# Kernel tuning notes

Measured on AMD Instinct MI355X. Metric: run time of the kernel, lower is better.

Reference implementation:

```python
import jax, jax.numpy as jnp
import numpy as np

NUM_HEADS = 12  # matches init_kwargs num_heads


def dwconv(x, w, b, groups):
    # depthwise conv, NHWC, SAME padding, stride 1 (DepthwiseConv2D in source)
    y = jax.lax.conv_general_dilated(x, w, (1, 1), 'SAME', (1, 1), (1, 1),
                                     ('NHWC', 'HWIO', 'NHWC'), groups)
    return y + b


def setup_inputs() -> dict:
    key = jax.random.key(0)
    ks = jax.random.split(key, 6)
    B, N, C = 16, 1025, 768  # N = 1 + 32*32
    inputs = jax.random.normal(ks[0], (B, N, C), jnp.float32)
    cpe_w = jax.random.normal(ks[1], (3, 3, 1, C), jnp.float32) * 0.05   # ConvPosEnc 3x3 depthwise
    cpe_b = jnp.zeros((C,), jnp.float32)
    w_qkv = jax.random.normal(ks[2], (C, 3 * C), jnp.float32) * 0.02     # Dense(dim*3, use_bias=False)
    crpe_w = jax.random.normal(ks[3], (1, 1, 1, C), jnp.float32) * 0.05  # ConvRelPosEnc window=1 depthwise
    crpe_b = jnp.zeros((C,), jnp.float32)
    w_proj = jax.random.normal(ks[4], (C, C), jnp.float32) * 0.02        # Dense(dim)
    b_proj = jnp.zeros((C,), jnp.float32)
    return {'inputs': inputs, 'cpe_w': cpe_w, 'cpe_b': cpe_b, 'w_qkv': w_qkv,
            'crpe_w': crpe_w, 'crpe_b': crpe_b, 'w_proj': w_proj, 'b_proj': b_proj}


def reference(inputs, cpe_w, cpe_b, w_qkv, crpe_w, crpe_b, w_proj, b_proj):
    B, N, C = inputs.shape
    H = W = int((N - 1) ** 0.5)
    nh = NUM_HEADS
    dh = C // nh
    scale = dh ** (-0.5)

    # ConvPosEnc: depthwise 3x3 conv on image tokens + residual, cls token passes through
    cls_tok, img = inputs[:, :1], inputs[:, 1:]
    feat = img.reshape(B, H, W, C)
    x = dwconv(feat, cpe_w, cpe_b, C) + feat
    pe = jnp.concatenate([cls_tok, x.reshape(B, H * W, C)], axis=1)  # [B,N,C]

    # qkv projection (no bias)
    qkv = (pe @ w_qkv).reshape(B, N, 3, nh, dh)
    qkv = jnp.transpose(qkv, (2, 0, 3, 1, 4))  # [3,B,nh,N,dh]
    q, k, v = qkv[0], qkv[1], qkv[2]

    # factorized (linear) attention: softmax over tokens on K, then two einsums
    k_soft = jax.nn.softmax(k, axis=2)
    kTv = jnp.einsum('bhnk,bhnv->bhkv', k_soft, v)       # [B,nh,dh,dh]
    factor_att = jnp.einsum('bhnk,bhkv->bhnv', q, kTv)   # [B,nh,N,dh]

    # ConvRelPosEnc (window_size=1): faithful to source including the raw reshapes
    q_img = q[:, :, 1:, :]                                # [B,nh,HW,dh]
    v_img = v[:, :, 1:, :].reshape(B, nh * dh, H, W)      # raw reshape as in source
    conv_v = dwconv(jnp.transpose(v_img, (0, 2, 3, 1)), crpe_w, crpe_b, C)  # NHWC
    conv_v = conv_v.reshape(B, nh, H * W, dh)             # raw reshape as in source
    ev_hat = jnp.concatenate([jnp.zeros((B, nh, 1, dh), q.dtype), q_img * conv_v], axis=2)

    # combine and project (source reshapes [B,nh,N,dh] directly to [B,N,C])
    out = (scale * factor_att + ev_hat).reshape(B, N, C)
    return out @ w_proj + b_proj
```

## Files before the change

kernel.cpp:

```cpp
#include <hip/hip_runtime.h>
#include <cstdint>

#define NH 12
#define CC 768
#define NN 1025
#define BB 16
#define HW 32
#define MPAD 16512
#define MV 16400

typedef _Float16 f16;
typedef _Float16 f16x4 __attribute__((ext_vector_type(4)));
typedef _Float16 f16x8 __attribute__((ext_vector_type(8)));
typedef float    f32x4 __attribute__((ext_vector_type(4)));

__device__ __forceinline__ f16 hi_part(float x) { return (f16)x; }
__device__ __forceinline__ f16 lo_part(float x) { f16 h = (f16)x; return (f16)(x - (float)h); }

template<int LO>
__global__ __launch_bounds__(192) void packA_cpe(const float* __restrict__ in,
                                                 const float* __restrict__ w,
                                                 const float* __restrict__ bias,
                                                 f16* __restrict__ Ah) {
    int m = blockIdx.x;
    int t = threadIdx.x;
    int c = t * 4;
    f16x4 o = {(f16)0, (f16)0, (f16)0, (f16)0};
    if (m < MV) {
        int b = m / NN, n = m % NN;
        float4 acc;
        if (n == 0) {
            acc = *(const float4*)(in + (size_t)m * CC + c);
        } else {
            int p = n - 1, y = p >> 5, x = p & 31;
            acc = *(const float4*)(bias + c);
            float4 ctr = *(const float4*)(in + (size_t)m * CC + c);
            acc.x += ctr.x; acc.y += ctr.y; acc.z += ctr.z; acc.w += ctr.w;
            #pragma unroll
            for (int ky = 0; ky < 3; ++ky) {
                int yy = y + ky - 1;
                if (yy < 0 || yy >= HW) continue;
                #pragma unroll
                for (int kx = 0; kx < 3; ++kx) {
                    int xx = x + kx - 1;
                    if (xx < 0 || xx >= HW) continue;
                    float4 wv = *(const float4*)(w + (size_t)(ky*3+kx)*CC + c);
                    float4 iv = *(const float4*)(in + ((size_t)(b*NN) + 1 + yy*HW + xx)*CC + c);
                    acc.x = fmaf(wv.x, iv.x, acc.x);
                    acc.y = fmaf(wv.y, iv.y, acc.y);
                    acc.z = fmaf(wv.z, iv.z, acc.z);
                    acc.w = fmaf(wv.w, iv.w, acc.w);
                }
            }
        }
        if (LO) { o[0]=lo_part(acc.x); o[1]=lo_part(acc.y); o[2]=lo_part(acc.z); o[3]=lo_part(acc.w); }
        else    { o[0]=hi_part(acc.x); o[1]=hi_part(acc.y); o[2]=hi_part(acc.z); o[3]=hi_part(acc.w); }
    }
    *(f16x4*)&Ah[(size_t)m * CC + c] = o;
}

template<int LO>
__global__ __launch_bounds__(192) void packA_attn(const float* __restrict__ qkv,
                                                  f16* __restrict__ Ah) {
    int m = blockIdx.x;
    int t = threadIdx.x;
    int c = t * 4;
    f16x4 o = {(f16)0, (f16)0, (f16)0, (f16)0};
    if (m < MV) {
        float4 v = *(const float4*)&qkv[(size_t)m * 2304 + 768 + c];
        if (LO) { o[0]=lo_part(v.x); o[1]=lo_part(v.y); o[2]=lo_part(v.z); o[3]=lo_part(v.w); }
        else    { o[0]=hi_part(v.x); o[1]=hi_part(v.y); o[2]=hi_part(v.z); o[3]=hi_part(v.w); }
    }
    *(f16x4*)&Ah[(size_t)m * CC + c] = o;
}

__global__ __launch_bounds__(256) void packBT(const float* __restrict__ W,
                                              f16* __restrict__ Bt, int Nc) {
    __shared__ float tile[32][33];
    int k0 = blockIdx.x * 32, n0 = blockIdx.y * 32;
    int t = threadIdx.x;
    int ty = t >> 3, tx4 = (t & 7) << 2;
    float4 v = *(const float4*)&W[(size_t)(k0 + ty) * Nc + n0 + tx4];
    tile[ty][tx4+0] = v.x; tile[ty][tx4+1] = v.y; tile[ty][tx4+2] = v.z; tile[ty][tx4+3] = v.w;
    __syncthreads();
    int nl = ty, kl = tx4;
    f16x4 oh, ol;
    #pragma unroll
    for (int i = 0; i < 4; ++i) {
        float x = tile[kl + i][nl];
        f16 h = (f16)x;
        oh[i] = h;
        ol[i] = (f16)(x - (float)h);
    }
    size_t base = (size_t)(n0 + nl) * 1536 + (k0 + kl);
    *(f16x4*)&Bt[base]       = oh;
    *(f16x4*)&Bt[base + 768] = ol;
}

template<int ACC>
__global__ __launch_bounds__(256) void gemm_mfma(const f16* __restrict__ A,
                                                 const f16* __restrict__ Bt,
                                                 const float* __restrict__ bias,
                                                 float* __restrict__ C,
                                                 int Nc, int nsteps, int boff1) {
    __shared__ f16 As[128][32];
    __shared__ f16 Bs[128][32];
    int t = threadIdx.x;
    int w = t >> 6, l = t & 63;
    int row0 = blockIdx.x * 128, col0 = blockIdx.y * 128;
    int wm = w >> 1, wn = w & 1;
    int r0 = t >> 2, kc0 = (t & 3) << 3;
    int r1 = 64 + r0;
    f32x4 zz = {0.f, 0.f, 0.f, 0.f};
    f32x4 acc[4][4];
    #pragma unroll
    for (int i = 0; i < 4; ++i)
        #pragma unroll
        for (int j = 0; j < 4; ++j) acc[i][j] = zz;

    for (int s = 0; s < nsteps; ++s) {
        int kk = (s % 24) * 32;
        int bo = (s < 24 ? 0 : boff1) + kk;
        const f16* Ag = A  + (size_t)row0 * 768  + kk;
        const f16* Bg = Bt + (size_t)col0 * 1536 + bo;
        f16x8 a0 = *(const f16x8*)(Ag + (size_t)r0 * 768  + kc0);
        f16x8 a1 = *(const f16x8*)(Ag + (size_t)r1 * 768  + kc0);
        f16x8 b0 = *(const f16x8*)(Bg + (size_t)r0 * 1536 + kc0);
        f16x8 b1 = *(const f16x8*)(Bg + (size_t)r1 * 1536 + kc0);
        __syncthreads();
        *(f16x8*)&As[r0][kc0] = a0;
        *(f16x8*)&As[r1][kc0] = a1;
        *(f16x8*)&Bs[r0][kc0] = b0;
        *(f16x8*)&Bs[r1][kc0] = b1;
        __syncthreads();
        f16x8 af[4], bf[4];
        #pragma unroll
        for (int i = 0; i < 4; ++i)
            af[i] = *(const f16x8*)&As[wm*64 + i*16 + (l & 15)][(l >> 4) * 8];
        #pragma unroll
        for (int j = 0; j < 4; ++j)
            bf[j] = *(const f16x8*)&Bs[wn*64 + j*16 + (l & 15)][(l >> 4) * 8];
        #pragma unroll
        for (int i = 0; i < 4; ++i)
            #pragma unroll
            for (int j = 0; j < 4; ++j)
                acc[i][j] = __builtin_amdgcn_mfma_f32_16x16x32_f16(af[i], bf[j], acc[i][j], 0, 0, 0);
    }
    #pragma unroll
    for (int i = 0; i < 4; ++i) {
        #pragma unroll
        for (int j = 0; j < 4; ++j) {
            int gc = col0 + wn*64 + j*16 + (l & 15);
            #pragma unroll
            for (int r = 0; r < 4; ++r) {
                int gr = row0 + wm*64 + i*16 + (l >> 4) * 4 + r;
                if (gr < MV) {
                    size_t off = (size_t)gr * Nc + gc;
                    float v = acc[i][j][r];
                    if (ACC) C[off] += v;
                    else     C[off] = bias ? v + bias[gc] : v;
                }
            }
        }
    }
}

__global__ __launch_bounds__(256) void kstats_kernel(const float* __restrict__ qkv,
                                                     float* __restrict__ kmax,
                                                     float* __restrict__ ksum) {
    int bh = blockIdx.x;
    int b = bh / NH, h = bh % NH;
    int t = threadIdx.x;
    int d = t & 63, slice = t >> 6;
    __shared__ float red[4][64];
    float m = -1e30f;
    for (int n = slice; n < NN; n += 4)
        m = fmaxf(m, qkv[(size_t)(b*NN + n)*2304 + 768 + h*64 + d]);
    red[slice][d] = m;
    __syncthreads();
    float mAll = fmaxf(fmaxf(red[0][d], red[1][d]), fmaxf(red[2][d], red[3][d]));
    __syncthreads();
    float s = 0.f;
    for (int n = slice; n < NN; n += 4)
        s += __expf(qkv[(size_t)(b*NN + n)*2304 + 768 + h*64 + d] - mAll);
    red[slice][d] = s;
    __syncthreads();
    if (slice == 0) {
        kmax[bh*64 + d] = mAll;
        ksum[bh*64 + d] = red[0][d] + red[1][d] + red[2][d] + red[3][d];
    }
}

__global__ __launch_bounds__(256) void ktv_kernel(const float* __restrict__ qkv,
                                                  const float* __restrict__ kmax,
                                                  const float* __restrict__ ksum,
                                                  float* __restrict__ kTv) {
    int bh = blockIdx.x;
    int b = bh / NH, h = bh % NH;
    int t = threadIdx.x;
    int d = t & 63, slice = t >> 6;
    __shared__ float sk[4][64];
    __shared__ float sv[4][64];
    __shared__ float smax[64];
    if (t < 64) smax[t] = kmax[bh*64 + t];
    __syncthreads();
    float acc[16] = {};
    int vg = slice * 16;
    for (int n0 = 0; n0 < NN; n0 += 4) {
        int n = n0 + slice;
        float ek = 0.f, vv = 0.f;
        if (n < NN) {
            const float* row = qkv + (size_t)(b*NN + n) * 2304;
            ek = __expf(row[768 + h*64 + d] - smax[d]);
            vv = row[1536 + h*64 + d];
        }
        sk[slice][d] = ek;
        sv[slice][d] = vv;
        __syncthreads();
        #pragma unroll
        for (int s = 0; s < 4; ++s) {
            float e = sk[s][d];
            #pragma unroll
            for (int j = 0; j < 16; ++j)
                acc[j] = fmaf(e, sv[s][vg + j], acc[j]);
        }
        __syncthreads();
    }
    float inv = 1.0f / ksum[bh*64 + d];
    #pragma unroll
    for (int j = 0; j < 16; ++j)
        kTv[(size_t)bh*4096 + (size_t)d*64 + vg + j] = acc[j] * inv;
}

__global__ __launch_bounds__(256) void attn_kernel(float* qkv,
                                                   const float* __restrict__ kTv,
                                                   const float* __restrict__ crpe_w,
                                                   const float* __restrict__ crpe_b) {
    int tile = blockIdx.x;
    int nt = tile % 65;
    int bh = tile / 65;
    int b = bh / NH, h = bh % NH;
    __shared__ float sKT[64][64];
    __shared__ float sq[16][68];
    int t = threadIdx.x;
    for (int i = t; i < 4096; i += 256)
        sKT[i >> 6][i & 63] = kTv[(size_t)bh*4096 + i];
    int tt = t >> 4;
    int dd = (t & 15) << 2;
    int n = nt * 16 + tt;
    float4 qv = make_float4(0,0,0,0);
    if (n < NN) qv = *(const float4*)(qkv + (size_t)(b*NN + n)*2304 + h*64 + dd);
    sq[tt][dd+0] = qv.x; sq[tt][dd+1] = qv.y;
    sq[tt][dd+2] = qv.z; sq[tt][dd+3] = qv.w;
    __syncthreads();
    float o0=0.f, o1=0.f, o2=0.f, o3=0.f;
    #pragma unroll
    for (int k = 0; k < 64; ++k) {
        float qk = sq[tt][k];
        float4 kt = *(const float4*)&sKT[k][dd];
        o0 = fmaf(qk, kt.x, o0); o1 = fmaf(qk, kt.y, o1);
        o2 = fmaf(qk, kt.z, o2); o3 = fmaf(qk, kt.w, o3);
    }
    if (n < NN) {
        float res[4] = {0.125f*o0, 0.125f*o1, 0.125f*o2, 0.125f*o3};
        if (n >= 1) {
            int np = n - 1;
            #pragma unroll
            for (int j = 0; j < 4; ++j) {
                int d = dd + j;
                int g = h*65536 + np*64 + d;
                int y = g / 24576;
                int r1 = g - y*24576;
                int x = r1 / 768;
                int c = r1 - x*768;
                int hs = c >> 6;
                int c64 = c & 63;
                int ns = c64*16 + (y >> 1);
                int ds = ((y & 1) << 5) + x;
                float vsrc = qkv[(size_t)(b*NN + 1 + ns)*2304 + 1536 + hs*64 + ds];
                float conv = fmaf(vsrc, crpe_w[c], crpe_b[c]);
                res[j] = fmaf(sq[tt][d], conv, res[j]);
            }
        }
        size_t f = (size_t)b*787200 + (size_t)h*65600 + (size_t)n*64 + dd;
        size_t adr = (f / 768) * 2304 + 768 + (f % 768);
        float4 r4 = make_float4(res[0], res[1], res[2], res[3]);
        *(float4*)&qkv[adr] = r4;
    }
}

extern "C" void kernel_launch(void* const* d_in, const int* in_sizes, int n_in,
                              void* d_out, int out_size, void* d_ws, size_t ws_size,
                              hipStream_t stream) {
    const float* inputs = (const float*)d_in[0];
    const float* cpe_w  = (const float*)d_in[1];
    const float* cpe_b  = (const float*)d_in[2];
    const float* w_qkv  = (const float*)d_in[3];
    const float* crpe_w = (const float*)d_in[4];
    const float* crpe_b = (const float*)d_in[5];
    const float* w_proj = (const float*)d_in[6];
    const float* b_proj = (const float*)d_in[7];
    float* out = (float*)d_out;
    float* ws  = (float*)d_ws;

    f16*   Ah   = (f16*)ws;
    float* qkv  = ws + 6340608;
    float* aux  = ws + 44126208;
    f16*   BpT1 = (f16*)aux;
    float* kTv  = aux;
    float* kmax = aux + 786432;
    float* ksum = aux + 798720;
    f16*   BpT2 = (f16*)(aux + 811008);

    packBT<<<dim3(24, 72), 256, 0, stream>>>(w_qkv, BpT1, 2304);
    packA_cpe<0><<<MPAD, 192, 0, stream>>>(inputs, cpe_w, cpe_b, Ah);
    gemm_mfma<0><<<dim3(129, 18), 256, 0, stream>>>(Ah, BpT1, nullptr, qkv, 2304, 48, 768);
    packA_cpe<1><<<MPAD, 192, 0, stream>>>(inputs, cpe_w, cpe_b, Ah);
    gemm_mfma<1><<<dim3(129, 18), 256, 0, stream>>>(Ah, BpT1, nullptr, qkv, 2304, 24, 0);

    kstats_kernel<<<BB*NH, 256, 0, stream>>>(qkv, kmax, ksum);
    ktv_kernel<<<BB*NH, 256, 0, stream>>>(qkv, kmax, ksum, kTv);
    attn_kernel<<<BB*NH*65, 256, 0, stream>>>(qkv, kTv, crpe_w, crpe_b);

    packBT<<<dim3(24, 24), 256, 0, stream>>>(w_proj, BpT2, 768);
    packA_attn<0><<<MPAD, 192, 0, stream>>>(qkv, Ah);
    gemm_mfma<0><<<dim3(129, 6), 256, 0, stream>>>(Ah, BpT2, b_proj, out, 768, 48, 768);
    packA_attn<1><<<MPAD, 192, 0, stream>>>(qkv, Ah);
    gemm_mfma<1><<<dim3(129, 6), 256, 0, stream>>>(Ah, BpT2, nullptr, out, 768, 24, 0);
}
```

Baseline: 1.119 ms.

## Double-buffer GEMM via direct global-to-LDS loads, swizzle tiles, split kTv reduction

The MFMA GEMM now loads tiles straight from global memory into LDS with global_load_lds and double-buffers them, so the next K-step's loads overlap the current MFMAs and one barrier per step is removed. It also switches to a 1D grid with an XCD-aware, grouped tile ordering meant to improve L2 reuse across blocks. Separately, the kTv reduction is split across 8 token chunks per head and combined with atomicAdd, with kstats zeroing the buffer first, to raise parallelism in a kernel that previously ran only 192 blocks. The cost is float atomic nondeterminism and more complex index math.

```diff
diff --git a/kernel.cpp b/kernel.cpp
--- a/kernel.cpp
+++ b/kernel.cpp
@@ -8,6 +8,7 @@
 #define HW 32
 #define MPAD 16512
 #define MV 16400
+#define GM 8
 
 typedef _Float16 f16;
 typedef _Float16 f16x4 __attribute__((ext_vector_type(4)));
@@ -16,6 +17,11 @@
 
 __device__ __forceinline__ f16 hi_part(float x) { return (f16)x; }
 __device__ __forceinline__ f16 lo_part(float x) { f16 h = (f16)x; return (f16)(x - (float)h); }
+
+__device__ __forceinline__ void gload16(const f16* g, f16* l) {
+    __builtin_amdgcn_global_load_lds((const __attribute__((address_space(1))) void*)g,
+                                     (__attribute__((address_space(3))) void*)l, 16, 0, 0);
+}
 
 template<int LO>
 __global__ __launch_bounds__(192) void packA_cpe(const float* __restrict__ in,
@@ -103,14 +109,31 @@
                                                  const float* __restrict__ bias,
                                                  float* __restrict__ C,
                                                  int Nc, int nsteps, int boff1) {
-    __shared__ f16 As[128][32];
-    __shared__ f16 Bs[128][32];
+    __shared__ f16 lds[16384];
     int t = threadIdx.x;
     int w = t >> 6, l = t & 63;
-    int row0 = blockIdx.x * 128, col0 = blockIdx.y * 128;
+
+    int nwg = gridDim.x;
+    int ntn = Nc >> 7;
+    int ntm = nwg / ntn;
+    int q8 = nwg >> 3, r8 = nwg & 7;
+    int xcd = blockIdx.x & 7, lin = blockIdx.x >> 3;
+    int wg = (xcd < r8 ? xcd * (q8 + 1) : r8 * (q8 + 1) + (xcd - r8) * q8) + lin;
+    int per_group = GM * ntn;
+    int g = wg / per_group, rem = wg - g * per_group;
+    int gmrows = ntm - g * GM; if (gmrows > GM) gmrows = GM;
+    int brow = g * GM + rem % gmrows;
+    int bcol = rem / gmrows;
+    int row0 = brow << 7, col0 = bcol << 7;
+
     int wm = w >> 1, wn = w & 1;
-    int r0 = t >> 2, kc0 = (t & 3) << 3;
-    int r1 = 64 + r0;
+
+    int srow = 32 * w + (l >> 2);
+    int achk = (l & 3) << 3;
+    const f16* Abase = A  + (size_t)(row0 + srow) * 768  + achk;
+    const f16* Bbase = Bt + (size_t)(col0 + srow) * 1536 + achk;
+    int lw = 32 * w * 32;
+
     f32x4 zz = {0.f, 0.f, 0.f, 0.f};
     f32x4 acc[4][4];
     #pragma unroll
@@ -118,34 +141,52 @@
         #pragma unroll
         for (int j = 0; j < 4; ++j) acc[i][j] = zz;
 
+    #define STAGE(bufi, kkv, bov)                                  \
+        {                                                          \
+            const f16* ga = Abase + (kkv);                         \
+            const f16* gb = Bbase + (bov);                         \
+            f16* la = &lds[(bufi)*8192 + lw];                      \
+            f16* lb = &lds[(bufi)*8192 + 4096 + lw];               \
+            gload16(ga,             la);                           \
+            gload16(ga + 16*768,    la + 512);                     \
+            gload16(gb,             lb);                           \
+            gload16(gb + 16*1536,   lb + 512);                     \
+        }
+
+    STAGE(0, 0, 0);
+    asm volatile("s_waitcnt vmcnt(0)" ::: "memory");
+    __syncthreads();
+
+    int buf = 0;
+    int rbA = wm * 64 + (l & 15);
+    int rbB = wn * 64 + (l & 15);
+    int coff = (l >> 4) << 3;
     for (int s = 0; s < nsteps; ++s) {
-        int kk = (s % 24) * 32;
-        int bo = (s < 24 ? 0 : boff1) + kk;
-        const f16* Ag = A  + (size_t)row0 * 768  + kk;
-        const f16* Bg = Bt + (size_t)col0 * 1536 + bo;
-        f16x8 a0 = *(const f16x8*)(Ag + (size_t)r0 * 768  + kc0);
-        f16x8 a1 = *(const f16x8*)(Ag + (size_t)r1 * 768  + kc0);
-        f16x8 b0 = *(const f16x8*)(Bg + (size_t)r0 * 1536 + kc0);
-        f16x8 b1 = *(const f16x8*)(Bg + (size_t)r1 * 1536 + kc0);
-        __syncthreads();
-        *(f16x8*)&As[r0][kc0] = a0;
-        *(f16x8*)&As[r1][kc0] = a1;
-        *(f16x8*)&Bs[r0][kc0] = b0;
-        *(f16x8*)&Bs[r1][kc0] = b1;
-        __syncthreads();
+        int sn = s + 1;
+        if (sn < nsteps) {
+            int kkn = (sn % 24) * 32;
+            int bon = (sn < 24 ? 0 : boff1) + kkn;
+            STAGE(buf ^ 1, kkn, bon);
+        }
+        const f16* Lb = &lds[buf * 8192];
         f16x8 af[4], bf[4];
         #pragma unroll
         for (int i = 0; i < 4; ++i)
-            af[i] = *(const f16x8*)&As[wm*64 + i*16 + (l & 15)][(l >> 4) * 8];
+            af[i] = *(const f16x8*)&Lb[(rbA + i*16) * 32 + coff];
         #pragma unroll
         for (int j = 0; j < 4; ++j)
-            bf[j] = *(const f16x8*)&Bs[wn*64 + j*16 + (l & 15)][(l >> 4) * 8];
+            bf[j] = *(const f16x8*)&Lb[4096 + (rbB + j*16) * 32 + coff];
         #pragma unroll
         for (int i = 0; i < 4; ++i)
             #pragma unroll
             for (int j = 0; j < 4; ++j)
                 acc[i][j] = __builtin_amdgcn_mfma_f32_16x16x32_f16(af[i], bf[j], acc[i][j], 0, 0, 0);
-    }
+        asm volatile("s_waitcnt vmcnt(0)" ::: "memory");
+        __syncthreads();
+        buf ^= 1;
+    }
+    #undef STAGE
+
     #pragma unroll
     for (int i = 0; i < 4; ++i) {
         #pragma unroll
@@ -167,10 +208,12 @@
 
 __global__ __launch_bounds__(256) void kstats_kernel(const float* __restrict__ qkv,
                                                      float* __restrict__ kmax,
-                                                     float* __restrict__ ksum) {
+                                                     float* __restrict__ ksum,
+                                                     float* __restrict__ kTv) {
     int bh = blockIdx.x;
     int b = bh / NH, h = bh % NH;
     int t = threadIdx.x;
+    for (int i = t; i < 4096; i += 256) kTv[(size_t)bh*4096 + i] = 0.f;
     int d = t & 63, slice = t >> 6;
     __shared__ float red[4][64];
     float m = -1e30f;
@@ -196,6 +239,7 @@
                                                   const float* __restrict__ ksum,
                                                   float* __restrict__ kTv) {
     int bh = blockIdx.x;
+    int chunk = blockIdx.y;
     int b = bh / NH, h = bh % NH;
     int t = threadIdx.x;
     int d = t & 63, slice = t >> 6;
@@ -206,10 +250,12 @@
     __syncthreads();
     float acc[16] = {};
     int vg = slice * 16;
-    for (int n0 = 0; n0 < NN; n0 += 4) {
+    int nstart = chunk * 128;
+    int nend = (chunk == 7) ? NN : (nstart + 128);
+    for (int n0 = nstart; n0 < nend; n0 += 4) {
         int n = n0 + slice;
         float ek = 0.f, vv = 0.f;
-        if (n < NN) {
+        if (n < nend) {
             const float* row = qkv + (size_t)(b*NN + n) * 2304;
             ek = __expf(row[768 + h*64 + d] - smax[d]);
             vv = row[1536 + h*64 + d];
@@ -229,7 +275,7 @@
     float inv = 1.0f / ksum[bh*64 + d];
     #pragma unroll
     for (int j = 0; j < 16; ++j)
-        kTv[(size_t)bh*4096 + (size_t)d*64 + vg + j] = acc[j] * inv;
+        atomicAdd(&kTv[(size_t)bh*4096 + (size_t)d*64 + vg + j], acc[j] * inv);
 }
 
 __global__ __launch_bounds__(256) void attn_kernel(float* qkv,
@@ -314,17 +360,17 @@
 
     packBT<<<dim3(24, 72), 256, 0, stream>>>(w_qkv, BpT1, 2304);
     packA_cpe<0><<<MPAD, 192, 0, stream>>>(inputs, cpe_w, cpe_b, Ah);
-    gemm_mfma<0><<<dim3(129, 18), 256, 0, stream>>>(Ah, BpT1, nullptr, qkv, 2304, 48, 768);
+    gemm_mfma<0><<<129*18, 256, 0, stream>>>(Ah, BpT1, nullptr, qkv, 2304, 48, 768);
     packA_cpe<1><<<MPAD, 192, 0, stream>>>(inputs, cpe_w, cpe_b, Ah);
-    gemm_mfma<1><<<dim3(129, 18), 256, 0, stream>>>(Ah, BpT1, nullptr, qkv, 2304, 24, 0);
-
-    kstats_kernel<<<BB*NH, 256, 0, stream>>>(qkv, kmax, ksum);
-    ktv_kernel<<<BB*NH, 256, 0, stream>>>(qkv, kmax, ksum, kTv);
+    gemm_mfma<1><<<129*18, 256, 0, stream>>>(Ah, BpT1, nullptr, qkv, 2304, 24, 0);
+
+    kstats_kernel<<<BB*NH, 256, 0, stream>>>(qkv, kmax, ksum, kTv);
+    ktv_kernel<<<dim3(BB*NH, 8), 256, 0, stream>>>(qkv, kmax, ksum, kTv);
     attn_kernel<<<BB*NH*65, 256, 0, stream>>>(qkv, kTv, crpe_w, crpe_b);
 
     packBT<<<dim3(24, 24), 256, 0, stream>>>(w_proj, BpT2, 768);
     packA_attn<0><<<MPAD, 192, 0, stream>>>(qkv, Ah);
-    gemm_mfma<0><<<dim3(129, 6), 256, 0, stream>>>(Ah, BpT2, b_proj, out, 768, 48, 768);
+    gemm_mfma<0><<<129*6, 256, 0, stream>>>(Ah, BpT2, b_proj, out, 768, 48, 768);
     packA_attn<1><<<MPAD, 192, 0, stream>>>(qkv, Ah);
-    gemm_mfma<1><<<dim3(129, 6), 256, 0, stream>>>(Ah, BpT2, nullptr, out, 768, 24, 0);
-}
+    gemm_mfma<1><<<129*6, 256, 0, stream>>>(Ah, BpT2, nullptr, out, 768, 24, 0);
+}
```

After: 1.213 ms. 8.4% more time.
